# Kernel tuning notes

Measured on AMD Instinct MI355X. Metric: run time of the kernel, lower is better.

The kernel has to match this reference:

```python
import jax, jax.numpy as jnp
import numpy as np

N = 4096      # sequence length (tokens)
D = 256       # model_dim
H = 4         # num_heads
DH = D // H   # dim_per_head = 64
TOPK = 30     # dot_attention default
SCALE = float((DH // H) ** -0.5)  # torch: (key.size(-1)//num_heads)**-0.5 = 16**-0.5 = 0.25
LN_EPS = 1e-5


def setup_inputs() -> dict:
    key = jax.random.key(0)
    ks = jax.random.split(key, 11)
    s = 0.02
    return {
        "key_in":   jax.random.normal(ks[0], (N, D), jnp.float32),
        "value_in": jax.random.normal(ks[1], (N, D), jnp.float32),
        "query_in": jax.random.normal(ks[2], (N, D), jnp.float32),
        "Wq": jax.random.normal(ks[3], (D, D), jnp.float32) * s,
        "bq": jax.random.normal(ks[4], (D,), jnp.float32) * s,
        "Wk": jax.random.normal(ks[5], (D, D), jnp.float32) * s,
        "bk": jax.random.normal(ks[6], (D,), jnp.float32) * s,
        "Wv": jax.random.normal(ks[7], (D, D), jnp.float32) * s,
        "bv": jax.random.normal(ks[8], (D,), jnp.float32) * s,
        "Wo": jax.random.normal(ks[9], (D, D), jnp.float32) * s,
        "bo": jax.random.normal(ks[10], (D,), jnp.float32) * s,
        "ln_g": jnp.ones((D,), jnp.float32),
        "ln_b": jnp.zeros((D,), jnp.float32),
    }


def reference(key_in, value_in, query_in, Wq, bq, Wk, bk, Wv, bv, Wo, bo, ln_g, ln_b):
    # Projections (nn.Linear: x @ W.T + b)
    q = query_in @ Wq.T + bq            # (N, D)
    k = key_in @ Wk.T + bk
    v = value_in @ Wv.T + bv
    # view(N, H, DH).transpose(0,1) -> (H, N, DH)
    qh = q.reshape(N, H, DH).transpose(1, 0, 2)
    kh = k.reshape(N, H, DH).transpose(1, 0, 2)
    vh = v.reshape(N, H, DH).transpose(1, 0, 2)

    scores = jnp.einsum('hnd,hmd->hnm', qh, kh) * SCALE   # (H, N, N)

    # top-k mask via scatter (faithful to torch.topk + scatter_)
    idx = jax.lax.top_k(scores, TOPK)[1]                  # (H, N, TOPK)
    mask = jnp.zeros_like(scores).at[
        jnp.arange(H)[:, None, None],
        jnp.arange(N)[None, :, None],
        idx].set(1.0)
    masked = jnp.where(mask > 0, scores, -jnp.inf)
    attn = jax.nn.softmax(masked, axis=-1)                # (H, N, N); dropout p=0 -> identity

    ctx = jnp.einsum('hnm,hmd->hnd', attn, vh)            # (H, N, DH)
    ctx = ctx.transpose(1, 0, 2).reshape(N, D)

    out = ctx @ Wo.T + bo
    resid = query_in + out                                # residual is pre-projection query
    mu = resid.mean(axis=-1, keepdims=True)
    var = resid.var(axis=-1, keepdims=True)               # biased var, like torch LayerNorm
    out = (resid - mu) / jnp.sqrt(var + LN_EPS) * ln_g + ln_b
    return out, attn
```

## Files before the change

kernel.cpp:

```cpp
#include <hip/hip_runtime.h>
#include <stdint.h>

#define N_TOK 4096
#define DIM   256
#define NH    4
#define DH    64
#define TOPK  30
#define CANDN 40
#define ATT_SCALE 0.25f
#define LN_EPS 1e-5f

typedef __attribute__((ext_vector_type(8))) short bf16x8;
typedef __attribute__((ext_vector_type(4))) float f32x4;

static __device__ __forceinline__ float bf2f(ushort u) {
    return __uint_as_float(((uint)u) << 16);
}
static __device__ __forceinline__ ushort f2bf(float f) {
    uint x = __float_as_uint(f);
    return (ushort)((x + 0x7FFFu + ((x >> 16) & 1u)) >> 16);
}
static __device__ __forceinline__ bf16x8 load_frag(const ushort* p) {
    union { int4 i; bf16x8 f; } u;
    u.i = *reinterpret_cast<const int4*>(p);
    return u.f;
}
static __device__ __forceinline__ uint s16key(uint u) {
    return (u & 0x8000u) ? (u ^ 0xFFFFu) : (u | 0x8000u);
}

#define BK 32
__global__ __launch_bounds__(256) void proj_gemm_f32(
    const float* __restrict__ A, const float* __restrict__ W,
    const float* __restrict__ bias, const float* __restrict__ addX,
    float* __restrict__ outF, ushort* __restrict__ outB)
{
    __shared__ float As[BK][64 + 4];
    __shared__ float Ws[BK][64 + 4];
    const int tid = threadIdx.x;
    const int tx = tid & 15;
    const int ty = tid >> 4;
    const int i0 = blockIdx.y * 64;
    const int j0 = blockIdx.x * 64;

    float acc[4][4];
#pragma unroll
    for (int r = 0; r < 4; r++)
#pragma unroll
        for (int c = 0; c < 4; c++) acc[r][c] = 0.f;

    for (int k0 = 0; k0 < DIM; k0 += BK) {
#pragma unroll
        for (int u = 0; u < 2; u++) {
            const int f = u * 256 + tid;
            const int r = f >> 3;
            const int c = (f & 7) * 4;
            float4 va = *reinterpret_cast<const float4*>(A + (size_t)(i0 + r) * DIM + k0 + c);
            As[c + 0][r] = va.x; As[c + 1][r] = va.y;
            As[c + 2][r] = va.z; As[c + 3][r] = va.w;
            float4 vw = *reinterpret_cast<const float4*>(W + (size_t)(j0 + r) * DIM + k0 + c);
            Ws[c + 0][r] = vw.x; Ws[c + 1][r] = vw.y;
            Ws[c + 2][r] = vw.z; Ws[c + 3][r] = vw.w;
        }
        __syncthreads();
#pragma unroll
        for (int kk = 0; kk < BK; kk++) {
            const float4 a4 = *reinterpret_cast<const float4*>(&As[kk][ty * 4]);
            const float4 b4 = *reinterpret_cast<const float4*>(&Ws[kk][tx * 4]);
            const float ar[4] = {a4.x, a4.y, a4.z, a4.w};
            const float br[4] = {b4.x, b4.y, b4.z, b4.w};
#pragma unroll
            for (int r = 0; r < 4; r++)
#pragma unroll
                for (int c = 0; c < 4; c++) acc[r][c] += ar[r] * br[c];
        }
        __syncthreads();
    }

#pragma unroll
    for (int r = 0; r < 4; r++) {
        const int gi = i0 + ty * 4 + r;
#pragma unroll
        for (int c = 0; c < 4; c++) {
            const int gj = j0 + tx * 4 + c;
            float v = acc[r][c] + bias[gj];
            if (addX) v += addX[(size_t)gi * DIM + gj];
            if (outF) outF[(size_t)gi * DIM + gj] = v;
            if (outB) outB[(size_t)gi * DIM + gj] = f2bf(v);
        }
    }
}

__global__ __launch_bounds__(256) void scores_kernel(
    const ushort* __restrict__ qb, const ushort* __restrict__ kb,
    ushort* __restrict__ sb)
{
    const int lane = threadIdx.x & 63;
    const int wv   = threadIdx.x >> 6;
    const int h    = blockIdx.z;
    const int i0   = blockIdx.y * 128 + wv * 32;
    const int j0   = blockIdx.x * 128;
    const int r = lane & 15, q = lane >> 4;
    const int koff = h * DH;

    f32x4 acc[2][8];
#pragma unroll
    for (int a = 0; a < 2; a++)
#pragma unroll
        for (int b = 0; b < 8; b++) acc[a][b] = (f32x4){0.f, 0.f, 0.f, 0.f};

#pragma unroll
    for (int ks = 0; ks < 2; ks++) {
        const int kk = koff + ks * 32 + q * 8;
        bf16x8 af[2], bfr[8];
#pragma unroll
        for (int mt = 0; mt < 2; mt++)
            af[mt] = load_frag(qb + (size_t)(i0 + mt * 16 + r) * DIM + kk);
#pragma unroll
        for (int jt = 0; jt < 8; jt++)
            bfr[jt] = load_frag(kb + (size_t)(j0 + jt * 16 + r) * DIM + kk);
#pragma unroll
        for (int mt = 0; mt < 2; mt++)
#pragma unroll
            for (int jt = 0; jt < 8; jt++)
                acc[mt][jt] = __builtin_amdgcn_mfma_f32_16x16x32_bf16(
                    af[mt], bfr[jt], acc[mt][jt], 0, 0, 0);
    }

#pragma unroll
    for (int mt = 0; mt < 2; mt++)
#pragma unroll
        for (int rg = 0; rg < 4; rg++) {
            const int gi = i0 + mt * 16 + q * 4 + rg;
            ushort* row = sb + ((size_t)(h * N_TOK + gi)) * N_TOK;
#pragma unroll
            for (int jt = 0; jt < 8; jt++)
                row[j0 + jt * 16 + r] = f2bf(acc[mt][jt][rg]);
        }
}

__global__ __launch_bounds__(64) void select_kernel(
    const ushort* __restrict__ sb, const float* __restrict__ qf,
    const float* __restrict__ kf, const float* __restrict__ vf,
    float* __restrict__ pval, int* __restrict__ pidx,
    float* __restrict__ ctx)
{
    const int lane = threadIdx.x;
    const int i = blockIdx.x, h = blockIdx.y;
    const int row = h * N_TOK + i;
    const ushort* srow = sb + (size_t)row * N_TOK;

    __shared__ __align__(16) float qsh[DH];
    __shared__ uint  cand[64];
    __shared__ uint  ccnt;
    __shared__ float pw[TOPK];
    __shared__ int   jw[TOPK];

    qsh[lane] = qf[(size_t)i * DIM + h * DH + lane];
    if (lane == 0) ccnt = 0;

    uint key[64];
    const int4* srow4 = reinterpret_cast<const int4*>(srow);
#pragma unroll
    for (int t = 0; t < 8; t++) {
        int4 cc = srow4[t * 64 + lane];
        uint w[4] = {(uint)cc.x, (uint)cc.y, (uint)cc.z, (uint)cc.w};
#pragma unroll
        for (int wi = 0; wi < 4; wi++) {
            key[t * 8 + wi * 2 + 0] = s16key(w[wi] & 0xFFFFu);
            key[t * 8 + wi * 2 + 1] = s16key(w[wi] >> 16);
        }
    }

    uint lo = 0;
#pragma unroll
    for (int b = 15; b >= 0; b--) {
        uint trial = lo | (1u << b);
        int c = 0;
#pragma unroll
        for (int s = 0; s < 64; s++) c += (key[s] >= trial) ? 1 : 0;
#pragma unroll
        for (int off = 32; off; off >>= 1) c += __shfl_xor(c, off);
        if (c >= CANDN) lo = trial;
    }

    __syncthreads();

#pragma unroll
    for (int t = 0; t < 8; t++)
#pragma unroll
        for (int e = 0; e < 8; e++) {
            if (key[t * 8 + e] >= lo) {
                uint pos = atomicAdd(&ccnt, 1u);
                if (pos < 64u) cand[pos] = (uint)(t * 512 + lane * 8 + e);
            }
        }
    __syncthreads();
    const int m = (int)min(ccnt, 64u);

    unsigned long long ukey = 0ull;
    if (lane < m) {
        const int j = (int)cand[lane];
        const float4* kr = reinterpret_cast<const float4*>(kf + (size_t)j * DIM + h * DH);
        const float4* qr = reinterpret_cast<const float4*>(qsh);
        float s = 0.f;
#pragma unroll
        for (int d = 0; d < 16; d++) {
            float4 a = qr[d], bb = kr[d];
            s += a.x * bb.x; s += a.y * bb.y; s += a.z * bb.z; s += a.w * bb.w;
        }
        uint bits = __float_as_uint(s);
        uint s32 = (bits & 0x80000000u) ? ~bits : (bits | 0x80000000u);
        ukey = ((unsigned long long)s32 << 12) | (unsigned long long)(4095 - j);
    }

#pragma unroll
    for (int k = 2; k <= 64; k <<= 1) {
#pragma unroll
        for (int jj = k >> 1; jj > 0; jj >>= 1) {
            unsigned long long o = __shfl_xor(ukey, jj);
            bool keepMax = ((lane & jj) != 0) ^ ((lane & k) != 0);
            ukey = keepMax ? (ukey > o ? ukey : o) : (ukey < o ? ukey : o);
        }
    }

    const int rank = 63 - lane;
    const int jsel = 4095 - (int)(ukey & 0xFFFull);
    uint s32b = (uint)(ukey >> 12);
    uint fb = (s32b & 0x80000000u) ? (s32b ^ 0x80000000u) : ~s32b;
    const float sc = __uint_as_float(fb);
    const float stop = __shfl(sc, 63);

    float e = (rank < TOPK) ? __expf((sc - stop) * ATT_SCALE) : 0.f;
    float esum = e;
#pragma unroll
    for (int off = 32; off; off >>= 1) esum += __shfl_xor(esum, off);
    const float p = e / esum;

    if (rank < TOPK) {
        pw[rank] = p; jw[rank] = jsel;
        pval[(size_t)row * 32 + rank] = p;
        pidx[(size_t)row * 32 + rank] = jsel;
    }
    __syncthreads();

    float a = 0.f;
#pragma unroll
    for (int c = 0; c < TOPK; c++)
        a += pw[c] * vf[(size_t)jw[c] * DIM + h * DH + lane];
    ctx[(size_t)i * DIM + h * DH + lane] = a;
}

__global__ __launch_bounds__(256) void attn_write(
    const float* __restrict__ pval, const int* __restrict__ pidx,
    float* __restrict__ attnF)
{
    const int r = blockIdx.x;
    float* rowp = attnF + (size_t)r * N_TOK;
    float4* row4 = reinterpret_cast<float4*>(rowp);
    const float4 z = {0.f, 0.f, 0.f, 0.f};
#pragma unroll
    for (int t = 0; t < 4; t++) row4[t * 256 + threadIdx.x] = z;
    __syncthreads();
    if (threadIdx.x < TOPK)
        rowp[pidx[(size_t)r * 32 + threadIdx.x]] = pval[(size_t)r * 32 + threadIdx.x];
}

__global__ __launch_bounds__(64) void ln_kernel(
    float* __restrict__ resb, const float* __restrict__ g,
    const float* __restrict__ b)
{
    const int i = blockIdx.x, lane = threadIdx.x;
    float4* rowp = reinterpret_cast<float4*>(resb + (size_t)i * DIM);
    float4 x = rowp[lane];
    float s  = x.x + x.y + x.z + x.w;
    float sq = x.x * x.x + x.y * x.y + x.z * x.z + x.w * x.w;
#pragma unroll
    for (int off = 32; off; off >>= 1) {
        s  += __shfl_xor(s, off);
        sq += __shfl_xor(sq, off);
    }
    const float mu  = s * (1.f / DIM);
    const float var = sq * (1.f / DIM) - mu * mu;
    const float rstd = rsqrtf(var + LN_EPS);
    const int col = lane * 4;
    float4 o;
    o.x = (x.x - mu) * rstd * g[col + 0] + b[col + 0];
    o.y = (x.y - mu) * rstd * g[col + 1] + b[col + 1];
    o.z = (x.z - mu) * rstd * g[col + 2] + b[col + 2];
    o.w = (x.w - mu) * rstd * g[col + 3] + b[col + 3];
    rowp[lane] = o;
}

extern "C" void kernel_launch(void* const* d_in, const int* in_sizes, int n_in,
                              void* d_out, int out_size, void* d_ws, size_t ws_size,
                              hipStream_t stream)
{
    const float* key_in   = (const float*)d_in[0];
    const float* value_in = (const float*)d_in[1];
    const float* query_in = (const float*)d_in[2];
    const float* Wq = (const float*)d_in[3];
    const float* bq = (const float*)d_in[4];
    const float* Wk = (const float*)d_in[5];
    const float* bk = (const float*)d_in[6];
    const float* Wv = (const float*)d_in[7];
    const float* bv = (const float*)d_in[8];
    const float* Wo = (const float*)d_in[9];
    const float* bo = (const float*)d_in[10];
    const float* ln_g = (const float*)d_in[11];
    const float* ln_b = (const float*)d_in[12];

    float* outF  = (float*)d_out;
    float* attnF = outF + (size_t)N_TOK * DIM;

    const size_t SC = 33554432;
    ushort* sb  = (ushort*)attnF;
    float*  qf  = attnF + SC;
    float*  kf  = attnF + SC + 1048576;
    float*  vf  = attnF + SC + 2097152;
    ushort* qb  = (ushort*)(attnF + SC + 3145728);
    ushort* kb  = (ushort*)(attnF + SC + 3670016);
    float*  ctx = attnF + SC + 4194304;

    float* pval = (float*)d_ws;
    int*   pidx = (int*)d_ws + 524288;

    const dim3 gP(4, 64), bP(256);
    proj_gemm_f32<<<gP, bP, 0, stream>>>(query_in, Wq, bq, nullptr, qf, qb);
    proj_gemm_f32<<<gP, bP, 0, stream>>>(key_in,   Wk, bk, nullptr, kf, kb);
    proj_gemm_f32<<<gP, bP, 0, stream>>>(value_in, Wv, bv, nullptr, vf, nullptr);

    scores_kernel<<<dim3(32, 32, NH), 256, 0, stream>>>(qb, kb, sb);
    select_kernel<<<dim3(N_TOK, NH), 64, 0, stream>>>(sb, qf, kf, vf, pval, pidx, ctx);

    proj_gemm_f32<<<gP, bP, 0, stream>>>(ctx, Wo, bo, query_in, outF, nullptr);
    ln_kernel<<<N_TOK, 64, 0, stream>>>(outF, ln_g, ln_b);

    attn_write<<<N_TOK * NH, 256, 0, stream>>>(pval, pidx, attnF);
}
```

Before: 535.2 us.

## Replace per-row bitwise radix select with LDS histogram threshold search

The scores kernel now stores order-preserving 16-bit keys, so the select step no longer converts each element. The 16-pass bitwise binary search for the candidate threshold becomes one max reduction, a 256-bin LDS histogram of distance-from-max, and a wave prefix scan to find the bin holding the 40th element. The old bisection is kept as a fallback when the threshold falls outside the histogram range. The select kernel also packs four rows per 256-thread block instead of one row per 64-thread block, at the cost of LDS atomic contention on the histogram.

```diff
diff --git a/kernel.cpp b/kernel.cpp
--- a/kernel.cpp
+++ b/kernel.cpp
@@ -13,9 +13,6 @@
 typedef __attribute__((ext_vector_type(8))) short bf16x8;
 typedef __attribute__((ext_vector_type(4))) float f32x4;
 
-static __device__ __forceinline__ float bf2f(ushort u) {
-    return __uint_as_float(((uint)u) << 16);
-}
 static __device__ __forceinline__ ushort f2bf(float f) {
     uint x = __float_as_uint(f);
     return (ushort)((x + 0x7FFFu + ((x >> 16) & 1u)) >> 16);
@@ -135,74 +132,130 @@
             ushort* row = sb + ((size_t)(h * N_TOK + gi)) * N_TOK;
 #pragma unroll
             for (int jt = 0; jt < 8; jt++)
-                row[j0 + jt * 16 + r] = f2bf(acc[mt][jt][rg]);
-        }
-}
-
-__global__ __launch_bounds__(64) void select_kernel(
+                row[j0 + jt * 16 + r] = (ushort)s16key(f2bf(acc[mt][jt][rg]));
+        }
+}
+
+__global__ __launch_bounds__(256) void select_kernel(
     const ushort* __restrict__ sb, const float* __restrict__ qf,
     const float* __restrict__ kf, const float* __restrict__ vf,
     float* __restrict__ pval, int* __restrict__ pidx,
     float* __restrict__ ctx)
 {
-    const int lane = threadIdx.x;
-    const int i = blockIdx.x, h = blockIdx.y;
-    const int row = h * N_TOK + i;
+    const int lane = threadIdx.x & 63;
+    const int wv   = threadIdx.x >> 6;
+    const int row  = blockIdx.x * 4 + wv;
+    const int h    = row >> 12;
+    const int i    = row & (N_TOK - 1);
     const ushort* srow = sb + (size_t)row * N_TOK;
 
-    __shared__ __align__(16) float qsh[DH];
-    __shared__ uint  cand[64];
-    __shared__ uint  ccnt;
-    __shared__ float pw[TOPK];
-    __shared__ int   jw[TOPK];
-
-    qsh[lane] = qf[(size_t)i * DIM + h * DH + lane];
-    if (lane == 0) ccnt = 0;
-
-    uint key[64];
+    __shared__ uint  hist[4][256];
+    __shared__ uint  cand[4][64];
+    __shared__ uint  ccnt[4];
+    __shared__ float pw[4][TOPK];
+    __shared__ int   jw[4][TOPK];
+    __shared__ __align__(16) float qsh[4][DH];
+
+    qsh[wv][lane] = qf[(size_t)i * DIM + h * DH + lane];
+    if (lane == 0) ccnt[wv] = 0;
+#pragma unroll
+    for (int b = 0; b < 4; b++) hist[wv][lane * 4 + b] = 0u;
+
+    uint kw[32];
     const int4* srow4 = reinterpret_cast<const int4*>(srow);
 #pragma unroll
     for (int t = 0; t < 8; t++) {
-        int4 cc = srow4[t * 64 + lane];
-        uint w[4] = {(uint)cc.x, (uint)cc.y, (uint)cc.z, (uint)cc.w};
-#pragma unroll
-        for (int wi = 0; wi < 4; wi++) {
-            key[t * 8 + wi * 2 + 0] = s16key(w[wi] & 0xFFFFu);
-            key[t * 8 + wi * 2 + 1] = s16key(w[wi] >> 16);
-        }
-    }
-
-    uint lo = 0;
-#pragma unroll
-    for (int b = 15; b >= 0; b--) {
-        uint trial = lo | (1u << b);
-        int c = 0;
-#pragma unroll
-        for (int s = 0; s < 64; s++) c += (key[s] >= trial) ? 1 : 0;
-#pragma unroll
-        for (int off = 32; off; off >>= 1) c += __shfl_xor(c, off);
-        if (c >= CANDN) lo = trial;
-    }
-
-    __syncthreads();
-
-#pragma unroll
-    for (int t = 0; t < 8; t++)
-#pragma unroll
-        for (int e = 0; e < 8; e++) {
-            if (key[t * 8 + e] >= lo) {
-                uint pos = atomicAdd(&ccnt, 1u);
-                if (pos < 64u) cand[pos] = (uint)(t * 512 + lane * 8 + e);
+        int4 c = srow4[t * 64 + lane];
+        kw[t * 4 + 0] = (uint)c.x; kw[t * 4 + 1] = (uint)c.y;
+        kw[t * 4 + 2] = (uint)c.z; kw[t * 4 + 3] = (uint)c.w;
+    }
+
+    uint mx = 0;
+#pragma unroll
+    for (int w = 0; w < 32; w++) {
+        uint lo16 = kw[w] & 0xFFFFu, hi16 = kw[w] >> 16;
+        mx = max(mx, max(lo16, hi16));
+    }
+#pragma unroll
+    for (int off = 32; off; off >>= 1)
+        mx = max(mx, (uint)__shfl_xor((int)mx, off));
+
+    __syncthreads();
+
+#pragma unroll
+    for (int w = 0; w < 32; w++) {
+        uint lo16 = kw[w] & 0xFFFFu, hi16 = kw[w] >> 16;
+        atomicAdd(&hist[wv][min(mx - lo16, 255u)], 1u);
+        atomicAdd(&hist[wv][min(mx - hi16, 255u)], 1u);
+    }
+    __syncthreads();
+
+    const uint c0 = hist[wv][lane * 4 + 0];
+    const uint c1 = hist[wv][lane * 4 + 1];
+    const uint c2 = hist[wv][lane * 4 + 2];
+    const uint c3 = hist[wv][lane * 4 + 3];
+    const uint seg = c0 + c1 + c2 + c3;
+    uint scan = seg;
+#pragma unroll
+    for (int d = 1; d < 64; d <<= 1) {
+        uint y = (uint)__shfl_up((int)scan, d);
+        if (lane >= d) scan += y;
+    }
+    const uint excl = scan - seg;
+    const bool crossing = (excl < CANDN) && (scan >= CANDN);
+    unsigned long long bal = __ballot(crossing);
+    const int srcLane = __ffsll(bal) - 1;
+    int tloc = lane * 4;
+    if (crossing) {
+        uint cum = excl + c0;
+        if (cum < CANDN) { tloc++; cum += c1;
+            if (cum < CANDN) { tloc++; cum += c2;
+                if (cum < CANDN) { tloc++; } } }
+    }
+    const int t = __shfl(tloc, srcLane);
+
+    uint T;
+    if (t < 255) {
+        T = mx - (uint)t;
+    } else {
+        uint lo = 0;
+#pragma unroll
+        for (int b = 15; b >= 0; b--) {
+            uint trial = lo | (1u << b);
+            int c = 0;
+#pragma unroll
+            for (int w = 0; w < 32; w++) {
+                c += ((kw[w] & 0xFFFFu) >= trial) ? 1 : 0;
+                c += ((kw[w] >> 16)     >= trial) ? 1 : 0;
             }
-        }
-    __syncthreads();
-    const int m = (int)min(ccnt, 64u);
+#pragma unroll
+            for (int off = 32; off; off >>= 1) c += __shfl_xor(c, off);
+            if (c >= CANDN) lo = trial;
+        }
+        T = lo;
+    }
+
+#pragma unroll
+    for (int w = 0; w < 32; w++) {
+        const uint lo16 = kw[w] & 0xFFFFu, hi16 = kw[w] >> 16;
+        const int jbase = (w >> 2) * 512 + lane * 8 + (w & 3) * 2;
+        if (lo16 >= T) {
+            uint pos = atomicAdd(&ccnt[wv], 1u);
+            if (pos < 64u) cand[wv][pos] = (uint)jbase;
+        }
+        if (hi16 >= T) {
+            uint pos = atomicAdd(&ccnt[wv], 1u);
+            if (pos < 64u) cand[wv][pos] = (uint)(jbase + 1);
+        }
+    }
+    __syncthreads();
+    const int m = (int)min(ccnt[wv], 64u);
 
     unsigned long long ukey = 0ull;
     if (lane < m) {
-        const int j = (int)cand[lane];
+        const int j = (int)cand[wv][lane];
         const float4* kr = reinterpret_cast<const float4*>(kf + (size_t)j * DIM + h * DH);
-        const float4* qr = reinterpret_cast<const float4*>(qsh);
+        const float4* qr = reinterpret_cast<const float4*>(qsh[wv]);
         float s = 0.f;
 #pragma unroll
         for (int d = 0; d < 16; d++) {
@@ -238,7 +291,7 @@
     const float p = e / esum;
 
     if (rank < TOPK) {
-        pw[rank] = p; jw[rank] = jsel;
+        pw[wv][rank] = p; jw[wv][rank] = jsel;
         pval[(size_t)row * 32 + rank] = p;
         pidx[(size_t)row * 32 + rank] = jsel;
     }
@@ -247,7 +300,7 @@
     float a = 0.f;
 #pragma unroll
     for (int c = 0; c < TOPK; c++)
-        a += pw[c] * vf[(size_t)jw[c] * DIM + h * DH + lane];
+        a += pw[wv][c] * vf[(size_t)jw[wv][c] * DIM + h * DH + lane];
     ctx[(size_t)i * DIM + h * DH + lane] = a;
 }
 
@@ -331,7 +384,7 @@
     proj_gemm_f32<<<gP, bP, 0, stream>>>(value_in, Wv, bv, nullptr, vf, nullptr);
 
     scores_kernel<<<dim3(32, 32, NH), 256, 0, stream>>>(qb, kb, sb);
-    select_kernel<<<dim3(N_TOK, NH), 64, 0, stream>>>(sb, qf, kf, vf, pval, pidx, ctx);
+    select_kernel<<<dim3(N_TOK * NH / 4), 256, 0, stream>>>(sb, qf, kf, vf, pval, pidx, ctx);
 
     proj_gemm_f32<<<gP, bP, 0, stream>>>(ctx, Wo, bo, query_in, outF, nullptr);
     ln_kernel<<<N_TOK, 64, 0, stream>>>(outF, ln_g, ln_b);
```

After: 638.6 us. 19.3% more time.
